# Kernel optimization log

Hardware: AMD Instinct MI355X
Metric: run time of the kernel (lower is better)

## Reference

```python
import jax, jax.numpy as jnp
import numpy as np

BN_EPS = 1e-5


def setup_inputs() -> dict:
    key = jax.random.key(0)
    k1, k2 = jax.random.split(key, 2)
    b, C, h, w = 4, 256, 64, 64
    K = 16  # num_codes is hard-coded to 16 inside __init__
    x = jax.random.normal(k1, (b, C, h, w), dtype=jnp.float32)
    conv_w = jax.random.normal(k2, (K, C), dtype=jnp.float32) * (1.0 / np.sqrt(C))
    bn_gamma = jnp.ones((K,), dtype=jnp.float32)
    bn_beta = jnp.zeros((K,), dtype=jnp.float32)
    return {"x": x, "conv_w": conv_w, "bn_gamma": bn_gamma, "bn_beta": bn_beta}


def reference(x, conv_w, bn_gamma, bn_beta):
    b, C, h, w = x.shape
    K = conv_w.shape[0]
    hw = h * w

    # 1x1 conv (no bias) -> BatchNorm2d (training-mode batch stats) -> ReLU
    cw = jnp.einsum('kc,bchw->bkhw', conv_w, x)          # (b, K, h, w)
    mean = cw.mean(axis=(0, 2, 3))                        # (K,)
    var = cw.var(axis=(0, 2, 3))                          # biased variance, (K,)
    cw = (cw - mean[None, :, None, None]) * jax.lax.rsqrt(var + BN_EPS)[None, :, None, None]
    cw = cw * bn_gamma[None, :, None, None] + bn_beta[None, :, None, None]
    cw = jax.nn.relu(cw)

    cw_flat = cw.reshape(b, K, hw)                        # (b, K, hw)
    scale = cw_flat.mean(axis=2)                          # (b, K)
    # Faithful to torch: flat row-major reinterpretation of (b,K,hw) as (b,hw,K,1)
    r = cw_flat.reshape(b, hw, K, 1)                      # (b, hw, K, 1)

    x2 = x.reshape(b, C, hw).transpose(0, 2, 1)           # (b, hw, C)
    diff = x2[:, :, None, :] - r                          # (b, hw, K, C)

    scaled_l2 = scale[:, :, None] * jnp.sum(diff * diff, axis=1)   # (b, K, C)
    aw = jax.nn.softmax(scaled_l2, axis=1)                # softmax over K, (b, K, C)
    encoded_feat = jnp.sum(aw[:, None, :, :] * diff, axis=1)       # (b, K, C)
    return encoded_feat
```

## Files before the change

### kernel.cpp

```cpp
#include <hip/hip_runtime.h>

#define BN_EPS 1e-5f

#define OFF_PBN     0
#define OFF_PSR     8192
#define OFF_PSX     24576
#define OFF_PSXX    155648
#define OFF_CROSSR  286720
#define OFF_CW      352256
#define OFF_PCX     614400
#define WS_NEED     ((size_t)(OFF_PCX + 2097152) * sizeof(float))

#define CONV_FMA(W, K0)                                  \
    acc[K0][0] = fmaf(W, xv.x, acc[K0][0]);              \
    acc[K0][1] = fmaf(W, xv.y, acc[K0][1]);              \
    acc[K0][2] = fmaf(W, xv.z, acc[K0][2]);              \
    acc[K0][3] = fmaf(W, xv.w, acc[K0][3]);

#define FMA16(v, rp)                                     \
    {                                                    \
        const float4* rq_ = (const float4*)(rp);         \
        float4 r0_ = rq_[0], r1_ = rq_[1];               \
        float4 r2_ = rq_[2], r3_ = rq_[3];               \
        acc[0]  = fmaf(v, r0_.x, acc[0]);                \
        acc[1]  = fmaf(v, r0_.y, acc[1]);                \
        acc[2]  = fmaf(v, r0_.z, acc[2]);                \
        acc[3]  = fmaf(v, r0_.w, acc[3]);                \
        acc[4]  = fmaf(v, r1_.x, acc[4]);                \
        acc[5]  = fmaf(v, r1_.y, acc[5]);                \
        acc[6]  = fmaf(v, r1_.z, acc[6]);                \
        acc[7]  = fmaf(v, r1_.w, acc[7]);                \
        acc[8]  = fmaf(v, r2_.x, acc[8]);                \
        acc[9]  = fmaf(v, r2_.y, acc[9]);                \
        acc[10] = fmaf(v, r2_.z, acc[10]);               \
        acc[11] = fmaf(v, r2_.w, acc[11]);               \
        acc[12] = fmaf(v, r3_.x, acc[12]);               \
        acc[13] = fmaf(v, r3_.y, acc[13]);               \
        acc[14] = fmaf(v, r3_.z, acc[14]);               \
        acc[15] = fmaf(v, r3_.w, acc[15]);               \
    }

__global__ __launch_bounds__(256, 2) void k_conv(const float* __restrict__ x,
                                                 const float* __restrict__ w,
                                                 float* __restrict__ cw,
                                                 float* __restrict__ pbn) {
    __shared__ float wlT[4124];
    __shared__ float bnl[4][32];
    int bid = blockIdx.x;
    int b   = bid >> 6;
    int ich = bid & 63;
    int t   = threadIdx.x;
    int cp  = t & 15;
    int il  = t >> 4;
    int wv  = t >> 6;

    for (int m = t; m < 4096; m += 256) {
        int k = m >> 8, c = m & 255;
        wlT[(c << 4) + ((c >> 5) << 2) + k] = w[m];
    }
    __syncthreads();

    float acc[16][4];
    #pragma unroll
    for (int k = 0; k < 16; ++k) {
        #pragma unroll
        for (int e = 0; e < 4; ++e) acc[k][e] = 0.f;
    }

    const float* xp = x + (size_t)(b * 256 + cp * 16) * 4096 + ich * 64 + il * 4;
    #pragma unroll
    for (int cc = 0; cc < 16; ++cc) {
        float4 xv = *(const float4*)(xp + (size_t)cc * 4096);
        int c = cp * 16 + cc;
        const float4* wr = (const float4*)&wlT[(c << 4) + ((c >> 5) << 2)];
        float4 w0 = wr[0], w1 = wr[1], w2 = wr[2], w3 = wr[3];
        CONV_FMA(w0.x, 0)  CONV_FMA(w0.y, 1)  CONV_FMA(w0.z, 2)  CONV_FMA(w0.w, 3)
        CONV_FMA(w1.x, 4)  CONV_FMA(w1.y, 5)  CONV_FMA(w1.z, 6)  CONV_FMA(w1.w, 7)
        CONV_FMA(w2.x, 8)  CONV_FMA(w2.y, 9)  CONV_FMA(w2.z, 10) CONV_FMA(w2.w, 11)
        CONV_FMA(w3.x, 12) CONV_FMA(w3.y, 13) CONV_FMA(w3.z, 14) CONV_FMA(w3.w, 15)
    }

    float r8[8][4];
    #pragma unroll
    for (int r = 0; r < 8; ++r) {
        #pragma unroll
        for (int e = 0; e < 4; ++e) {
            float lo = acc[r][e]     + __shfl_xor(acc[r][e], 1);
            float hi = acc[r + 8][e] + __shfl_xor(acc[r + 8][e], 1);
            r8[r][e] = (cp & 1) ? hi : lo;
        }
    }
    float r4v[4][4];
    #pragma unroll
    for (int r = 0; r < 4; ++r) {
        #pragma unroll
        for (int e = 0; e < 4; ++e) {
            float lo = r8[r][e]     + __shfl_xor(r8[r][e], 2);
            float hi = r8[r + 4][e] + __shfl_xor(r8[r + 4][e], 2);
            r4v[r][e] = (cp & 2) ? hi : lo;
        }
    }
    float r2[2][4];
    #pragma unroll
    for (int r = 0; r < 2; ++r) {
        #pragma unroll
        for (int e = 0; e < 4; ++e) {
            float lo = r4v[r][e]     + __shfl_xor(r4v[r][e], 4);
            float hi = r4v[r + 2][e] + __shfl_xor(r4v[r + 2][e], 4);
            r2[r][e] = (cp & 4) ? hi : lo;
        }
    }
    float r1[4];
    #pragma unroll
    for (int e = 0; e < 4; ++e) {
        float lo = r2[0][e] + __shfl_xor(r2[0][e], 8);
        float hi = r2[1][e] + __shfl_xor(r2[1][e], 8);
        r1[e] = (cp & 8) ? hi : lo;
    }
    int ko = ((cp & 1) << 3) | (((cp >> 1) & 1) << 2) | (((cp >> 2) & 1) << 1)
           | ((cp >> 3) & 1);

    float4 st;
    st.x = r1[0]; st.y = r1[1]; st.z = r1[2]; st.w = r1[3];
    *(float4*)(cw + (size_t)b * 65536 + (size_t)ko * 4096 + ich * 64 + il * 4) = st;

    float s1 = r1[0] + r1[1] + r1[2] + r1[3];
    float s2 = r1[0]*r1[0] + r1[1]*r1[1] + r1[2]*r1[2] + r1[3]*r1[3];
    #pragma unroll
    for (int m = 16; m <= 32; m <<= 1) {
        s1 += __shfl_xor(s1, m);
        s2 += __shfl_xor(s2, m);
    }
    if ((t & 48) == 0) { bnl[wv][ko] = s1; bnl[wv][16 + ko] = s2; }
    __syncthreads();
    if (t < 32) {
        pbn[bid * 32 + t] = bnl[0][t] + bnl[1][t] + bnl[2][t] + bnl[3][t];
    }
}

template <bool PCX>
__global__ __launch_bounds__(256, 2) void k_main(const float* __restrict__ x,
                                                 const float* __restrict__ gamma,
                                                 const float* __restrict__ beta,
                                                 float* __restrict__ ws,
                                                 float* __restrict__ pcx) {
    __shared__ float xl[8192];
    __shared__ float rl[512];
    __shared__ float red1[256], red2[256];
    __shared__ float bnred[256];
    int bid = blockIdx.x;
    int b   = bid >> 7;
    int s   = bid & 127;
    int kp  = s >> 3;
    int t   = threadIdx.x;

    {
        int col = t & 31, row0 = t >> 5;
        float p = 0.f;
        for (int m = row0; m < 256; m += 8) p += ws[OFF_PBN + m * 32 + col];
        bnred[t] = p;
    }
    __syncthreads();
    float s1 = 0.f, s2 = 0.f;
    #pragma unroll
    for (int j = 0; j < 8; ++j) {
        s1 += bnred[j * 32 + kp];
        s2 += bnred[j * 32 + 16 + kp];
    }
    float mean = s1 * (1.f / 16384.f);
    float var  = s2 * (1.f / 16384.f) - mean * mean;
    float aa   = gamma[kp] * rsqrtf(var + BN_EPS);
    float bb   = beta[kp] - mean * aa;

    #pragma unroll
    for (int j = 0; j < 8; ++j) {
        int F  = j * 256 + t;
        int cc = F >> 3, i4 = F & 7;
        const float* pa = x + (size_t)(b * 256 + cc) * 4096 + s * 32 + i4 * 4;
        float4 v = *(const float4*)pa;
        int ib = i4 * 4;
        xl[(ib + 0) * 256 + (cc ^ (ib + 0))] = v.x;
        xl[(ib + 1) * 256 + (cc ^ (ib + 1))] = v.y;
        xl[(ib + 2) * 256 + (cc ^ (ib + 2))] = v.z;
        xl[(ib + 3) * 256 + (cc ^ (ib + 3))] = v.w;
    }

    const float* cwp = ws + OFF_CW + (size_t)b * 65536 + (size_t)kp * 4096
                     + (size_t)(s & 7) * 512;
    float sr = 0.f, srr = 0.f;
    #pragma unroll
    for (int j = 0; j < 2; ++j) {
        float v = cwp[t + j * 256];
        v = fmaxf(fmaf(v, aa, bb), 0.f);
        rl[t + j * 256] = v;
        sr += v; srr += v * v;
    }
    red1[t] = sr; red2[t] = srr;
    __syncthreads();

    if (t < 16) {
        float a1 = 0.f, a2 = 0.f;
        for (int m = t; m < 256; m += 16) { a1 += red1[m]; a2 += red2[m]; }
        ws[OFF_PSR + bid * 32 + t]      = a1;
        ws[OFF_PSR + bid * 32 + 16 + t] = a2;
    }

    int c = t;
    float acc[16];
    #pragma unroll
    for (int k = 0; k < 16; ++k) acc[k] = 0.f;
    float xs = 0.f, xs2 = 0.f;
    #pragma unroll
    for (int ii = 0; ii < 32; ++ii) {
        float xv = xl[ii * 256 + (c ^ ii)];
        xs += xv; xs2 += xv * xv;
        FMA16(xv, rl + ii * 16);
    }

    ws[OFF_PSX  + bid * 256 + c] = xs;
    ws[OFF_PSXX + bid * 256 + c] = xs2;
    if (PCX) {
        float* pp = pcx + (size_t)(bid * 16) * 256 + c;
        #pragma unroll
        for (int k = 0; k < 16; ++k) pp[(size_t)k * 256] = acc[k];
    } else {
        #pragma unroll
        for (int k = 0; k < 16; ++k)
            atomicAdd(ws + OFF_CROSSR + (b * 16 + k) * 256 + c, acc[k]);
    }
}

__global__ __launch_bounds__(256) void k_red(const float* __restrict__ pcx,
                                             float* __restrict__ crossr) {
    int bid = blockIdx.x;
    int b  = bid >> 6;
    int k  = (bid >> 2) & 15;
    int sg = bid & 3;
    int c  = threadIdx.x;
    float acc = 0.f;
    #pragma unroll 8
    for (int m = 0; m < 32; ++m) {
        int sl = sg * 32 + m;
        acc += pcx[(size_t)((b * 128 + sl) * 16 + k) * 256 + c];
    }
    crossr[((sg * 4 + b) * 16 + k) * 256 + c] = acc;
}

__global__ __launch_bounds__(256) void k_final(const float* __restrict__ ws,
                                               float* __restrict__ out) {
    __shared__ float srl[4096];
    __shared__ float fin[48];
    int b = blockIdx.x;
    int t = threadIdx.x;

    const float* psr = ws + OFF_PSR + (size_t)b * 128 * 32;
    #pragma unroll
    for (int j = 0; j < 16; ++j) srl[j * 256 + t] = psr[j * 256 + t];
    __syncthreads();

    if (t < 16) {
        float v = 0.f;
        for (int s = 0; s < 128; ++s) v += srl[s * 32 + t];
        fin[t] = v;
    } else if (t < 32) {
        int k = t - 16;
        float v = 0.f;
        for (int s = 0; s < 128; ++s) v += srl[s * 32 + 16 + k];
        fin[16 + k] = v;
    } else if (t < 48) {
        int kp = t - 32;
        float v = 0.f;
        for (int s = kp * 8; s < kp * 8 + 8; ++s)
            for (int k2 = 0; k2 < 16; ++k2) v += srl[s * 32 + k2];
        fin[32 + kp] = v;
    }
    __syncthreads();

    int c = t;
    float sx = 0.f, sxx = 0.f;
    const float* psx  = ws + OFF_PSX  + (size_t)b * 128 * 256;
    const float* psxx = ws + OFF_PSXX + (size_t)b * 128 * 256;
    for (int p = 0; p < 128; ++p) {
        sx  += psx[p * 256 + c];
        sxx += psxx[p * 256 + c];
    }

    float sl2[16];
    float mx = -1e30f;
    #pragma unroll
    for (int k = 0; k < 16; ++k) {
        float cr = 0.f;
        #pragma unroll
        for (int sg = 0; sg < 4; ++sg)
            cr += ws[OFF_CROSSR + ((sg * 4 + b) * 16 + k) * 256 + c];
        float v = fin[32 + k] * (1.f / 4096.f) * (sxx - 2.f * cr + fin[16 + k]);
        sl2[k] = v;
        mx = fmaxf(mx, v);
    }
    float den = 0.f;
    #pragma unroll
    for (int k = 0; k < 16; ++k) {
        float e = __expf(sl2[k] - mx);
        sl2[k] = e;
        den += e;
    }
    float inv = 1.f / den;
    #pragma unroll
    for (int k = 0; k < 16; ++k)
        out[(size_t)(b * 16 + k) * 256 + c] = sl2[k] * inv * (sx - fin[k]);
}

extern "C" void kernel_launch(void* const* d_in, const int* in_sizes, int n_in,
                              void* d_out, int out_size, void* d_ws, size_t ws_size,
                              hipStream_t stream) {
    const float* x     = (const float*)d_in[0];
    const float* w     = (const float*)d_in[1];
    const float* gamma = (const float*)d_in[2];
    const float* beta  = (const float*)d_in[3];
    float* ws  = (float*)d_ws;
    float* out = (float*)d_out;

    bool use_pcx = ws_size >= WS_NEED;

    k_conv<<<256, 256, 0, stream>>>(x, w, ws + OFF_CW, ws + OFF_PBN);
    if (use_pcx) {
        k_main<true><<<512, 256, 0, stream>>>(x, gamma, beta, ws, ws + OFF_PCX);
        k_red<<<256, 256, 0, stream>>>(ws + OFF_PCX, ws + OFF_CROSSR);
    } else {
        hipMemsetAsync(ws + OFF_CROSSR, 0, 65536 * sizeof(float), stream);
        k_main<false><<<512, 256, 0, stream>>>(x, gamma, beta, ws, nullptr);
    }
    k_final<<<4, 256, 0, stream>>>(ws, out);
}
```

Measured before the change: 102.3 us.

## Double thread count in conv and main kernels, move sx reduction into k_red

Runs k_conv and k_main with 512 threads per block. In k_conv each thread now handles 8 channels with all x loads issued up front, and a shared-memory cross-wave reduction replaces part of the shuffle tree. k_main splits the 32 spatial positions into two halves per channel and writes twice as many partial sums. The per-channel sx/sxx reductions move from the single-wave k_final into the parallel k_red, and the BN-stat reduction in k_main now runs after the x tile loads are issued, so the global loads overlap. In exchange the workspace and the partial-sum traffic double.

```diff
diff --git a/kernel.cpp b/kernel.cpp
--- a/kernel.cpp
+++ b/kernel.cpp
@@ -5,17 +5,18 @@
 #define OFF_PBN     0
 #define OFF_PSR     8192
 #define OFF_PSX     24576
-#define OFF_PSXX    155648
-#define OFF_CROSSR  286720
-#define OFF_CW      352256
-#define OFF_PCX     614400
-#define WS_NEED     ((size_t)(OFF_PCX + 2097152) * sizeof(float))
-
-#define CONV_FMA(W, K0)                                  \
-    acc[K0][0] = fmaf(W, xv.x, acc[K0][0]);              \
-    acc[K0][1] = fmaf(W, xv.y, acc[K0][1]);              \
-    acc[K0][2] = fmaf(W, xv.z, acc[K0][2]);              \
-    acc[K0][3] = fmaf(W, xv.w, acc[K0][3]);
+#define OFF_PSXX    286720
+#define OFF_CROSSR  548864
+#define OFF_SXF     614400
+#define OFF_CW      622592
+#define OFF_PCX     884736
+#define WS_NEED     ((size_t)(OFF_PCX + 4194304) * sizeof(float))
+
+#define CONV_FMA(W, K0, XV)                              \
+    acc[K0][0] = fmaf(W, XV.x, acc[K0][0]);              \
+    acc[K0][1] = fmaf(W, XV.y, acc[K0][1]);              \
+    acc[K0][2] = fmaf(W, XV.z, acc[K0][2]);              \
+    acc[K0][3] = fmaf(W, XV.w, acc[K0][3]);
 
 #define FMA16(v, rp)                                     \
     {                                                    \
@@ -40,25 +41,30 @@
         acc[15] = fmaf(v, r3_.w, acc[15]);               \
     }
 
-__global__ __launch_bounds__(256, 2) void k_conv(const float* __restrict__ x,
-                                                 const float* __restrict__ w,
+__global__ __launch_bounds__(512, 2) void k_conv(const float* __restrict__ x,
+                                                 const float* __restrict__ wq,
                                                  float* __restrict__ cw,
                                                  float* __restrict__ pbn) {
-    __shared__ float wlT[4124];
-    __shared__ float bnl[4][32];
+    __shared__ float wlT[4224];
+    __shared__ float wred[8 * 1088];
     int bid = blockIdx.x;
     int b   = bid >> 6;
     int ich = bid & 63;
     int t   = threadIdx.x;
-    int cp  = t & 15;
-    int il  = t >> 4;
+    int il  = t & 15;
+    int cp  = t >> 4;
     int wv  = t >> 6;
 
-    for (int m = t; m < 4096; m += 256) {
+    for (int m = t; m < 4096; m += 512) {
         int k = m >> 8, c = m & 255;
-        wlT[(c << 4) + ((c >> 5) << 2) + k] = w[m];
-    }
-    __syncthreads();
+        wlT[c * 16 + (c >> 3) * 4 + k] = wq[m];
+    }
+    __syncthreads();
+
+    float4 xv[8];
+    const float* xp = x + (size_t)(b * 256 + cp * 8) * 4096 + ich * 64 + il * 4;
+    #pragma unroll
+    for (int cc = 0; cc < 8; ++cc) xv[cc] = *(const float4*)(xp + (size_t)cc * 4096);
 
     float acc[16][4];
     #pragma unroll
@@ -67,17 +73,19 @@
         for (int e = 0; e < 4; ++e) acc[k][e] = 0.f;
     }
 
-    const float* xp = x + (size_t)(b * 256 + cp * 16) * 4096 + ich * 64 + il * 4;
-    #pragma unroll
-    for (int cc = 0; cc < 16; ++cc) {
-        float4 xv = *(const float4*)(xp + (size_t)cc * 4096);
-        int c = cp * 16 + cc;
-        const float4* wr = (const float4*)&wlT[(c << 4) + ((c >> 5) << 2)];
+    #pragma unroll
+    for (int cc = 0; cc < 8; ++cc) {
+        int c = cp * 8 + cc;
+        const float4* wr = (const float4*)&wlT[c * 16 + (c >> 3) * 4];
         float4 w0 = wr[0], w1 = wr[1], w2 = wr[2], w3 = wr[3];
-        CONV_FMA(w0.x, 0)  CONV_FMA(w0.y, 1)  CONV_FMA(w0.z, 2)  CONV_FMA(w0.w, 3)
-        CONV_FMA(w1.x, 4)  CONV_FMA(w1.y, 5)  CONV_FMA(w1.z, 6)  CONV_FMA(w1.w, 7)
-        CONV_FMA(w2.x, 8)  CONV_FMA(w2.y, 9)  CONV_FMA(w2.z, 10) CONV_FMA(w2.w, 11)
-        CONV_FMA(w3.x, 12) CONV_FMA(w3.y, 13) CONV_FMA(w3.z, 14) CONV_FMA(w3.w, 15)
+        CONV_FMA(w0.x, 0,  xv[cc]) CONV_FMA(w0.y, 1,  xv[cc])
+        CONV_FMA(w0.z, 2,  xv[cc]) CONV_FMA(w0.w, 3,  xv[cc])
+        CONV_FMA(w1.x, 4,  xv[cc]) CONV_FMA(w1.y, 5,  xv[cc])
+        CONV_FMA(w1.z, 6,  xv[cc]) CONV_FMA(w1.w, 7,  xv[cc])
+        CONV_FMA(w2.x, 8,  xv[cc]) CONV_FMA(w2.y, 9,  xv[cc])
+        CONV_FMA(w2.z, 10, xv[cc]) CONV_FMA(w2.w, 11, xv[cc])
+        CONV_FMA(w3.x, 12, xv[cc]) CONV_FMA(w3.y, 13, xv[cc])
+        CONV_FMA(w3.z, 14, xv[cc]) CONV_FMA(w3.w, 15, xv[cc])
     }
 
     float r8[8][4];
@@ -85,61 +93,57 @@
     for (int r = 0; r < 8; ++r) {
         #pragma unroll
         for (int e = 0; e < 4; ++e) {
-            float lo = acc[r][e]     + __shfl_xor(acc[r][e], 1);
-            float hi = acc[r + 8][e] + __shfl_xor(acc[r + 8][e], 1);
+            float lo = acc[r][e]     + __shfl_xor(acc[r][e], 16);
+            float hi = acc[r + 8][e] + __shfl_xor(acc[r + 8][e], 16);
             r8[r][e] = (cp & 1) ? hi : lo;
         }
     }
-    float r4v[4][4];
+    float r4[4][4];
     #pragma unroll
     for (int r = 0; r < 4; ++r) {
         #pragma unroll
         for (int e = 0; e < 4; ++e) {
-            float lo = r8[r][e]     + __shfl_xor(r8[r][e], 2);
-            float hi = r8[r + 4][e] + __shfl_xor(r8[r + 4][e], 2);
-            r4v[r][e] = (cp & 2) ? hi : lo;
-        }
-    }
-    float r2[2][4];
-    #pragma unroll
-    for (int r = 0; r < 2; ++r) {
-        #pragma unroll
-        for (int e = 0; e < 4; ++e) {
-            float lo = r4v[r][e]     + __shfl_xor(r4v[r][e], 4);
-            float hi = r4v[r + 2][e] + __shfl_xor(r4v[r + 2][e], 4);
-            r2[r][e] = (cp & 4) ? hi : lo;
-        }
-    }
-    float r1[4];
-    #pragma unroll
-    for (int e = 0; e < 4; ++e) {
-        float lo = r2[0][e] + __shfl_xor(r2[0][e], 8);
-        float hi = r2[1][e] + __shfl_xor(r2[1][e], 8);
-        r1[e] = (cp & 8) ? hi : lo;
-    }
-    int ko = ((cp & 1) << 3) | (((cp >> 1) & 1) << 2) | (((cp >> 2) & 1) << 1)
-           | ((cp >> 3) & 1);
-
-    float4 st;
-    st.x = r1[0]; st.y = r1[1]; st.z = r1[2]; st.w = r1[3];
-    *(float4*)(cw + (size_t)b * 65536 + (size_t)ko * 4096 + ich * 64 + il * 4) = st;
-
-    float s1 = r1[0] + r1[1] + r1[2] + r1[3];
-    float s2 = r1[0]*r1[0] + r1[1]*r1[1] + r1[2]*r1[2] + r1[3]*r1[3];
-    #pragma unroll
-    for (int m = 16; m <= 32; m <<= 1) {
-        s1 += __shfl_xor(s1, m);
-        s2 += __shfl_xor(s2, m);
-    }
-    if ((t & 48) == 0) { bnl[wv][ko] = s1; bnl[wv][16 + ko] = s2; }
-    __syncthreads();
-    if (t < 32) {
-        pbn[bid * 32 + t] = bnl[0][t] + bnl[1][t] + bnl[2][t] + bnl[3][t];
+            float lo = r8[r][e]     + __shfl_xor(r8[r][e], 32);
+            float hi = r8[r + 4][e] + __shfl_xor(r8[r + 4][e], 32);
+            r4[r][e] = (cp & 2) ? hi : lo;
+        }
+    }
+    int ko = (cp & 1) * 8 + ((cp >> 1) & 1) * 4;
+    #pragma unroll
+    for (int j = 0; j < 4; ++j) {
+        float4 v;
+        v.x = r4[j][0]; v.y = r4[j][1]; v.z = r4[j][2]; v.w = r4[j][3];
+        *(float4*)&wred[wv * 1088 + il * 68 + (ko + j) * 4] = v;
+    }
+    __syncthreads();
+
+    if (t < 256) {
+        int k = t >> 4, ilo = t & 15;
+        float4 s;
+        s.x = 0.f; s.y = 0.f; s.z = 0.f; s.w = 0.f;
+        #pragma unroll
+        for (int w8 = 0; w8 < 8; ++w8) {
+            float4 v = *(const float4*)&wred[w8 * 1088 + ilo * 68 + k * 4];
+            s.x += v.x; s.y += v.y; s.z += v.z; s.w += v.w;
+        }
+        *(float4*)(cw + (size_t)b * 65536 + (size_t)k * 4096 + ich * 64 + ilo * 4) = s;
+
+        float s1 = s.x + s.y + s.z + s.w;
+        float s2 = s.x * s.x + s.y * s.y + s.z * s.z + s.w * s.w;
+        #pragma unroll
+        for (int m = 1; m <= 8; m <<= 1) {
+            s1 += __shfl_xor(s1, m);
+            s2 += __shfl_xor(s2, m);
+        }
+        if (ilo == 0) {
+            pbn[bid * 32 + k]      = s1;
+            pbn[bid * 32 + 16 + k] = s2;
+        }
     }
 }
 
 template <bool PCX>
-__global__ __launch_bounds__(256, 2) void k_main(const float* __restrict__ x,
+__global__ __launch_bounds__(512, 2) void k_main(const float* __restrict__ x,
                                                  const float* __restrict__ gamma,
                                                  const float* __restrict__ beta,
                                                  float* __restrict__ ws,
@@ -153,28 +157,12 @@
     int s   = bid & 127;
     int kp  = s >> 3;
     int t   = threadIdx.x;
-
-    {
-        int col = t & 31, row0 = t >> 5;
-        float p = 0.f;
-        for (int m = row0; m < 256; m += 8) p += ws[OFF_PBN + m * 32 + col];
-        bnred[t] = p;
-    }
-    __syncthreads();
-    float s1 = 0.f, s2 = 0.f;
-    #pragma unroll
-    for (int j = 0; j < 8; ++j) {
-        s1 += bnred[j * 32 + kp];
-        s2 += bnred[j * 32 + 16 + kp];
-    }
-    float mean = s1 * (1.f / 16384.f);
-    float var  = s2 * (1.f / 16384.f) - mean * mean;
-    float aa   = gamma[kp] * rsqrtf(var + BN_EPS);
-    float bb   = beta[kp] - mean * aa;
-
-    #pragma unroll
-    for (int j = 0; j < 8; ++j) {
-        int F  = j * 256 + t;
+    int c   = t & 255;
+    int ih  = t >> 8;
+
+    #pragma unroll
+    for (int j = 0; j < 4; ++j) {
+        int F  = j * 512 + t;
         int cc = F >> 3, i4 = F & 7;
         const float* pa = x + (size_t)(b * 256 + cc) * 4096 + s * 32 + i4 * 4;
         float4 v = *(const float4*)pa;
@@ -185,19 +173,37 @@
         xl[(ib + 3) * 256 + (cc ^ (ib + 3))] = v.w;
     }
 
-    const float* cwp = ws + OFF_CW + (size_t)b * 65536 + (size_t)kp * 4096
-                     + (size_t)(s & 7) * 512;
-    float sr = 0.f, srr = 0.f;
-    #pragma unroll
-    for (int j = 0; j < 2; ++j) {
-        float v = cwp[t + j * 256];
-        v = fmaxf(fmaf(v, aa, bb), 0.f);
-        rl[t + j * 256] = v;
-        sr += v; srr += v * v;
-    }
-    red1[t] = sr; red2[t] = srr;
-    __syncthreads();
-
+    if (t < 256) {
+        int col = t & 31, row0 = t >> 5;
+        float p = 0.f;
+        for (int m = row0; m < 256; m += 8) p += ws[OFF_PBN + m * 32 + col];
+        bnred[t] = p;
+    }
+    __syncthreads();
+    float s1 = 0.f, s2 = 0.f;
+    #pragma unroll
+    for (int j = 0; j < 8; ++j) {
+        s1 += bnred[j * 32 + kp];
+        s2 += bnred[j * 32 + 16 + kp];
+    }
+    float mean = s1 * (1.f / 16384.f);
+    float var  = s2 * (1.f / 16384.f) - mean * mean;
+    float aa   = gamma[kp] * rsqrtf(var + BN_EPS);
+    float bb   = beta[kp] - mean * aa;
+
+    {
+        float v = ws[OFF_CW + (size_t)b * 65536 + (size_t)kp * 4096
+                     + (size_t)(s & 7) * 512 + t];
+        rl[t] = fmaxf(fmaf(v, aa, bb), 0.f);
+    }
+    __syncthreads();
+
+    if (t < 256) {
+        float v1 = rl[t], v2 = rl[t + 256];
+        red1[t] = v1 + v2;
+        red2[t] = v1 * v1 + v2 * v2;
+    }
+    __syncthreads();
     if (t < 16) {
         float a1 = 0.f, a2 = 0.f;
         for (int m = t; m < 256; m += 16) { a1 += red1[m]; a2 += red2[m]; }
@@ -205,33 +211,35 @@
         ws[OFF_PSR + bid * 32 + 16 + t] = a2;
     }
 
-    int c = t;
     float acc[16];
     #pragma unroll
     for (int k = 0; k < 16; ++k) acc[k] = 0.f;
     float xs = 0.f, xs2 = 0.f;
     #pragma unroll
-    for (int ii = 0; ii < 32; ++ii) {
-        float xv = xl[ii * 256 + (c ^ ii)];
-        xs += xv; xs2 += xv * xv;
-        FMA16(xv, rl + ii * 16);
-    }
-
-    ws[OFF_PSX  + bid * 256 + c] = xs;
-    ws[OFF_PSXX + bid * 256 + c] = xs2;
+    for (int q = 0; q < 16; ++q) {
+        int ii = ih * 16 + q;
+        float xvv = xl[ii * 256 + (c ^ ii)];
+        xs += xvv; xs2 += xvv * xvv;
+        FMA16(xvv, rl + ii * 16);
+    }
+
+    ws[OFF_PSX  + (size_t)(bid * 2 + ih) * 256 + c] = xs;
+    ws[OFF_PSXX + (size_t)(bid * 2 + ih) * 256 + c] = xs2;
     if (PCX) {
-        float* pp = pcx + (size_t)(bid * 16) * 256 + c;
+        float* pp = pcx + (size_t)((bid * 2 + ih) * 16) * 256 + c;
         #pragma unroll
         for (int k = 0; k < 16; ++k) pp[(size_t)k * 256] = acc[k];
     } else {
         #pragma unroll
         for (int k = 0; k < 16; ++k)
-            atomicAdd(ws + OFF_CROSSR + (b * 16 + k) * 256 + c, acc[k]);
+            atomicAdd(ws + OFF_CROSSR + ((0 * 4 + b) * 16 + k) * 256 + c, acc[k]);
+        atomicAdd(ws + OFF_SXF + (size_t)(b * 8 + 0) * 256 + c, xs);
+        atomicAdd(ws + OFF_SXF + (size_t)(b * 8 + 1) * 256 + c, xs2);
     }
 }
 
 __global__ __launch_bounds__(256) void k_red(const float* __restrict__ pcx,
-                                             float* __restrict__ crossr) {
+                                             float* __restrict__ ws) {
     int bid = blockIdx.x;
     int b  = bid >> 6;
     int k  = (bid >> 2) & 15;
@@ -239,11 +247,25 @@
     int c  = threadIdx.x;
     float acc = 0.f;
     #pragma unroll 8
-    for (int m = 0; m < 32; ++m) {
-        int sl = sg * 32 + m;
-        acc += pcx[(size_t)((b * 128 + sl) * 16 + k) * 256 + c];
-    }
-    crossr[((sg * 4 + b) * 16 + k) * 256 + c] = acc;
+    for (int j = 0; j < 64; ++j) {
+        int r = sg * 64 + j;
+        acc += pcx[(size_t)((b * 256 + r) * 16 + k) * 256 + c];
+    }
+    ws[OFF_CROSSR + ((sg * 4 + b) * 16 + k) * 256 + c] = acc;
+
+    if (k == 0) {
+        float sxq = 0.f;
+        #pragma unroll 8
+        for (int j = 0; j < 64; ++j)
+            sxq += ws[OFF_PSX + (size_t)(b * 256 + sg * 64 + j) * 256 + c];
+        ws[OFF_SXF + (size_t)((b * 4 + sg) * 2 + 0) * 256 + c] = sxq;
+    } else if (k == 1) {
+        float sxxq = 0.f;
+        #pragma unroll 8
+        for (int j = 0; j < 64; ++j)
+            sxxq += ws[OFF_PSXX + (size_t)(b * 256 + sg * 64 + j) * 256 + c];
+        ws[OFF_SXF + (size_t)((b * 4 + sg) * 2 + 1) * 256 + c] = sxxq;
+    }
 }
 
 __global__ __launch_bounds__(256) void k_final(const float* __restrict__ ws,
@@ -278,11 +300,10 @@
 
     int c = t;
     float sx = 0.f, sxx = 0.f;
-    const float* psx  = ws + OFF_PSX  + (size_t)b * 128 * 256;
-    const float* psxx = ws + OFF_PSXX + (size_t)b * 128 * 256;
-    for (int p = 0; p < 128; ++p) {
-        sx  += psx[p * 256 + c];
-        sxx += psxx[p * 256 + c];
+    #pragma unroll
+    for (int sg = 0; sg < 4; ++sg) {
+        sx  += ws[OFF_SXF + (size_t)((b * 4 + sg) * 2 + 0) * 256 + c];
+        sxx += ws[OFF_SXF + (size_t)((b * 4 + sg) * 2 + 1) * 256 + c];
     }
 
     float sl2[16];
@@ -293,7 +314,9 @@
         #pragma unroll
         for (int sg = 0; sg < 4; ++sg)
             cr += ws[OFF_CROSSR + ((sg * 4 + b) * 16 + k) * 256 + c];
-        float v = fin[32 + k] * (1.f / 4096.f) * (sxx - 2.f * cr + fin[16 + k]);
+        float sc  = fin[32 + k] * (1.f / 4096.f);
+        float srr = fin[16 + k];
+        float v = sc * (sxx - 2.f * cr + srr);
         sl2[k] = v;
         mx = fmaxf(mx, v);
     }
@@ -306,8 +329,10 @@
     }
     float inv = 1.f / den;
     #pragma unroll
-    for (int k = 0; k < 16; ++k)
-        out[(size_t)(b * 16 + k) * 256 + c] = sl2[k] * inv * (sx - fin[k]);
+    for (int k = 0; k < 16; ++k) {
+        float srk = fin[k];
+        out[(size_t)(b * 16 + k) * 256 + c] = sl2[k] * inv * (sx - srk);
+    }
 }
 
 extern "C" void kernel_launch(void* const* d_in, const int* in_sizes, int n_in,
@@ -322,13 +347,14 @@
 
     bool use_pcx = ws_size >= WS_NEED;
 
-    k_conv<<<256, 256, 0, stream>>>(x, w, ws + OFF_CW, ws + OFF_PBN);
+    k_conv<<<256, 512, 0, stream>>>(x, w, ws + OFF_CW, ws + OFF_PBN);
     if (use_pcx) {
-        k_main<true><<<512, 256, 0, stream>>>(x, gamma, beta, ws, ws + OFF_PCX);
-        k_red<<<256, 256, 0, stream>>>(ws + OFF_PCX, ws + OFF_CROSSR);
+        k_main<true><<<512, 512, 0, stream>>>(x, gamma, beta, ws, ws + OFF_PCX);
+        k_red<<<256, 256, 0, stream>>>(ws + OFF_PCX, ws);
     } else {
-        hipMemsetAsync(ws + OFF_CROSSR, 0, 65536 * sizeof(float), stream);
-        k_main<false><<<512, 256, 0, stream>>>(x, gamma, beta, ws, nullptr);
+        hipMemsetAsync(ws + OFF_CROSSR, 0,
+                       (OFF_CW - OFF_CROSSR) * sizeof(float), stream);
+        k_main<false><<<512, 512, 0, stream>>>(x, gamma, beta, ws, nullptr);
     }
     k_final<<<4, 256, 0, stream>>>(ws, out);
 }
```

Result: no change. 103.5 us (+1.2%).

## Fuse all stages into one persistent kernel with global atomic barriers

Applied to the files above, without the earlier changes.

Replaces the four separate kernel launches (conv, main, reduce, final) with a single 512-block kernel that separates the phases with software grid barriers built on agent-scope atomics. The x tile is loaded into LDS before the conv phase so its latency overlaps the conv work, and the final sx/sxx reduction is split across extra blocks. The aim is to remove launch gaps and the tail of the serial small kernels. The risks are that the spin barriers deadlock unless all 512 blocks are co-resident, and that the fallback for a too-small workspace is removed.

```diff
diff --git a/kernel.cpp b/kernel.cpp
--- a/kernel.cpp
+++ b/kernel.cpp
@@ -7,9 +7,11 @@
 #define OFF_PSX     24576
 #define OFF_PSXX    155648
 #define OFF_CROSSR  286720
-#define OFF_CW      352256
-#define OFF_PCX     614400
-#define WS_NEED     ((size_t)(OFF_PCX + 2097152) * sizeof(float))
+#define OFF_FIN     352256
+#define OFF_SXF     352512
+#define OFF_CW      356608
+#define OFF_PCX     618752
+#define OFF_BAR     2715904
 
 #define CONV_FMA(W, K0)                                  \
     acc[K0][0] = fmaf(W, xv.x, acc[K0][0]);              \
@@ -40,274 +42,300 @@
         acc[15] = fmaf(v, r3_.w, acc[15]);               \
     }
 
-__global__ __launch_bounds__(256, 2) void k_conv(const float* __restrict__ x,
-                                                 const float* __restrict__ w,
-                                                 float* __restrict__ cw,
-                                                 float* __restrict__ pbn) {
-    __shared__ float wlT[4124];
-    __shared__ float bnl[4][32];
+__device__ __forceinline__ void gbar(unsigned* cnt, unsigned target) {
+    __syncthreads();
+    if (threadIdx.x == 0) {
+        __threadfence();
+        __hip_atomic_fetch_add(cnt, 1u, __ATOMIC_ACQ_REL, __HIP_MEMORY_SCOPE_AGENT);
+        while (__hip_atomic_load(cnt, __ATOMIC_ACQUIRE, __HIP_MEMORY_SCOPE_AGENT)
+               < target)
+            __builtin_amdgcn_s_sleep(2);
+        __threadfence();
+    }
+    __syncthreads();
+}
+
+__global__ __launch_bounds__(256, 2) void k_all(const float* __restrict__ x,
+                                                const float* __restrict__ w,
+                                                const float* __restrict__ gamma,
+                                                const float* __restrict__ beta,
+                                                float* __restrict__ ws,
+                                                float* __restrict__ out) {
+    __shared__ float lds[12448];
+    unsigned* bar = (unsigned*)( nullptr);
+    float* xl = lds;
     int bid = blockIdx.x;
-    int b   = bid >> 6;
-    int ich = bid & 63;
     int t   = threadIdx.x;
-    int cp  = t & 15;
-    int il  = t >> 4;
-    int wv  = t >> 6;
-
-    for (int m = t; m < 4096; m += 256) {
-        int k = m >> 8, c = m & 255;
-        wlT[(c << 4) + ((c >> 5) << 2) + k] = w[m];
-    }
-    __syncthreads();
-
-    float acc[16][4];
-    #pragma unroll
-    for (int k = 0; k < 16; ++k) {
-        #pragma unroll
-        for (int e = 0; e < 4; ++e) acc[k][e] = 0.f;
-    }
-
-    const float* xp = x + (size_t)(b * 256 + cp * 16) * 4096 + ich * 64 + il * 4;
-    #pragma unroll
-    for (int cc = 0; cc < 16; ++cc) {
-        float4 xv = *(const float4*)(xp + (size_t)cc * 4096);
-        int c = cp * 16 + cc;
-        const float4* wr = (const float4*)&wlT[(c << 4) + ((c >> 5) << 2)];
-        float4 w0 = wr[0], w1 = wr[1], w2 = wr[2], w3 = wr[3];
-        CONV_FMA(w0.x, 0)  CONV_FMA(w0.y, 1)  CONV_FMA(w0.z, 2)  CONV_FMA(w0.w, 3)
-        CONV_FMA(w1.x, 4)  CONV_FMA(w1.y, 5)  CONV_FMA(w1.z, 6)  CONV_FMA(w1.w, 7)
-        CONV_FMA(w2.x, 8)  CONV_FMA(w2.y, 9)  CONV_FMA(w2.z, 10) CONV_FMA(w2.w, 11)
-        CONV_FMA(w3.x, 12) CONV_FMA(w3.y, 13) CONV_FMA(w3.z, 14) CONV_FMA(w3.w, 15)
-    }
-
-    float r8[8][4];
-    #pragma unroll
-    for (int r = 0; r < 8; ++r) {
+    bar = (unsigned*)(ws + OFF_BAR);
+
+    {
+        int b = bid >> 7;
+        int s = bid & 127;
+        #pragma unroll
+        for (int j = 0; j < 8; ++j) {
+            int F  = j * 256 + t;
+            int cc = F >> 3, i4 = F & 7;
+            const float* pa = x + (size_t)(b * 256 + cc) * 4096 + s * 32 + i4 * 4;
+            float4 v = *(const float4*)pa;
+            int ib = i4 * 4;
+            xl[(ib + 0) * 256 + (cc ^ (ib + 0))] = v.x;
+            xl[(ib + 1) * 256 + (cc ^ (ib + 1))] = v.y;
+            xl[(ib + 2) * 256 + (cc ^ (ib + 2))] = v.z;
+            xl[(ib + 3) * 256 + (cc ^ (ib + 3))] = v.w;
+        }
+    }
+
+    if (bid < 256) {
+        float* wlT = lds + 8192;
+        float* bnl = lds + 8192 + 4124;
+        int b   = bid >> 6;
+        int ich = bid & 63;
+        int cp  = t & 15;
+        int il  = t >> 4;
+        int wv  = t >> 6;
+
+        for (int m = t; m < 4096; m += 256) {
+            int k = m >> 8, c = m & 255;
+            wlT[(c << 4) + ((c >> 5) << 2) + k] = w[m];
+        }
+        __syncthreads();
+
+        float acc[16][4];
+        #pragma unroll
+        for (int k = 0; k < 16; ++k) {
+            #pragma unroll
+            for (int e = 0; e < 4; ++e) acc[k][e] = 0.f;
+        }
+
+        const float* xp = x + (size_t)(b * 256 + cp * 16) * 4096 + ich * 64 + il * 4;
+        #pragma unroll
+        for (int cc = 0; cc < 16; ++cc) {
+            float4 xv = *(const float4*)(xp + (size_t)cc * 4096);
+            int c = cp * 16 + cc;
+            const float4* wr = (const float4*)&wlT[(c << 4) + ((c >> 5) << 2)];
+            float4 w0 = wr[0], w1 = wr[1], w2 = wr[2], w3 = wr[3];
+            CONV_FMA(w0.x, 0)  CONV_FMA(w0.y, 1)  CONV_FMA(w0.z, 2)  CONV_FMA(w0.w, 3)
+            CONV_FMA(w1.x, 4)  CONV_FMA(w1.y, 5)  CONV_FMA(w1.z, 6)  CONV_FMA(w1.w, 7)
+            CONV_FMA(w2.x, 8)  CONV_FMA(w2.y, 9)  CONV_FMA(w2.z, 10) CONV_FMA(w2.w, 11)
+            CONV_FMA(w3.x, 12) CONV_FMA(w3.y, 13) CONV_FMA(w3.z, 14) CONV_FMA(w3.w, 15)
+        }
+
+        float r8[8][4];
+        #pragma unroll
+        for (int r = 0; r < 8; ++r) {
+            #pragma unroll
+            for (int e = 0; e < 4; ++e) {
+                float lo = acc[r][e]     + __shfl_xor(acc[r][e], 1);
+                float hi = acc[r + 8][e] + __shfl_xor(acc[r + 8][e], 1);
+                r8[r][e] = (cp & 1) ? hi : lo;
+            }
+        }
+        float r4v[4][4];
+        #pragma unroll
+        for (int r = 0; r < 4; ++r) {
+            #pragma unroll
+            for (int e = 0; e < 4; ++e) {
+                float lo = r8[r][e]     + __shfl_xor(r8[r][e], 2);
+                float hi = r8[r + 4][e] + __shfl_xor(r8[r + 4][e], 2);
+                r4v[r][e] = (cp & 2) ? hi : lo;
+            }
+        }
+        float r2[2][4];
+        #pragma unroll
+        for (int r = 0; r < 2; ++r) {
+            #pragma unroll
+            for (int e = 0; e < 4; ++e) {
+                float lo = r4v[r][e]     + __shfl_xor(r4v[r][e], 4);
+                float hi = r4v[r + 2][e] + __shfl_xor(r4v[r + 2][e], 4);
+                r2[r][e] = (cp & 4) ? hi : lo;
+            }
+        }
+        float r1[4];
         #pragma unroll
         for (int e = 0; e < 4; ++e) {
-            float lo = acc[r][e]     + __shfl_xor(acc[r][e], 1);
-            float hi = acc[r + 8][e] + __shfl_xor(acc[r + 8][e], 1);
-            r8[r][e] = (cp & 1) ? hi : lo;
-        }
-    }
-    float r4v[4][4];
-    #pragma unroll
-    for (int r = 0; r < 4; ++r) {
-        #pragma unroll
-        for (int e = 0; e < 4; ++e) {
-            float lo = r8[r][e]     + __shfl_xor(r8[r][e], 2);
-            float hi = r8[r + 4][e] + __shfl_xor(r8[r + 4][e], 2);
-            r4v[r][e] = (cp & 2) ? hi : lo;
-        }
-    }
-    float r2[2][4];
-    #pragma unroll
-    for (int r = 0; r < 2; ++r) {
-        #pragma unroll
-        for (int e = 0; e < 4; ++e) {
-            float lo = r4v[r][e]     + __shfl_xor(r4v[r][e], 4);
-            float hi = r4v[r + 2][e] + __shfl_xor(r4v[r + 2][e], 4);
-            r2[r][e] = (cp & 4) ? hi : lo;
-        }
-    }
-    float r1[4];
-    #pragma unroll
-    for (int e = 0; e < 4; ++e) {
-        float lo = r2[0][e] + __shfl_xor(r2[0][e], 8);
-        float hi = r2[1][e] + __shfl_xor(r2[1][e], 8);
-        r1[e] = (cp & 8) ? hi : lo;
-    }
-    int ko = ((cp & 1) << 3) | (((cp >> 1) & 1) << 2) | (((cp >> 2) & 1) << 1)
-           | ((cp >> 3) & 1);
-
-    float4 st;
-    st.x = r1[0]; st.y = r1[1]; st.z = r1[2]; st.w = r1[3];
-    *(float4*)(cw + (size_t)b * 65536 + (size_t)ko * 4096 + ich * 64 + il * 4) = st;
-
-    float s1 = r1[0] + r1[1] + r1[2] + r1[3];
-    float s2 = r1[0]*r1[0] + r1[1]*r1[1] + r1[2]*r1[2] + r1[3]*r1[3];
-    #pragma unroll
-    for (int m = 16; m <= 32; m <<= 1) {
-        s1 += __shfl_xor(s1, m);
-        s2 += __shfl_xor(s2, m);
-    }
-    if ((t & 48) == 0) { bnl[wv][ko] = s1; bnl[wv][16 + ko] = s2; }
-    __syncthreads();
-    if (t < 32) {
-        pbn[bid * 32 + t] = bnl[0][t] + bnl[1][t] + bnl[2][t] + bnl[3][t];
-    }
-}
-
-template <bool PCX>
-__global__ __launch_bounds__(256, 2) void k_main(const float* __restrict__ x,
-                                                 const float* __restrict__ gamma,
-                                                 const float* __restrict__ beta,
-                                                 float* __restrict__ ws,
-                                                 float* __restrict__ pcx) {
-    __shared__ float xl[8192];
-    __shared__ float rl[512];
-    __shared__ float red1[256], red2[256];
-    __shared__ float bnred[256];
-    int bid = blockIdx.x;
-    int b   = bid >> 7;
-    int s   = bid & 127;
-    int kp  = s >> 3;
-    int t   = threadIdx.x;
+            float lo = r2[0][e] + __shfl_xor(r2[0][e], 8);
+            float hi = r2[1][e] + __shfl_xor(r2[1][e], 8);
+            r1[e] = (cp & 8) ? hi : lo;
+        }
+        int ko = ((cp & 1) << 3) | (((cp >> 1) & 1) << 2) | (((cp >> 2) & 1) << 1)
+               | ((cp >> 3) & 1);
+
+        float4 st;
+        st.x = r1[0]; st.y = r1[1]; st.z = r1[2]; st.w = r1[3];
+        *(float4*)(ws + OFF_CW + (size_t)b * 65536 + (size_t)ko * 4096
+                   + ich * 64 + il * 4) = st;
+
+        float s1 = r1[0] + r1[1] + r1[2] + r1[3];
+        float s2 = r1[0]*r1[0] + r1[1]*r1[1] + r1[2]*r1[2] + r1[3]*r1[3];
+        #pragma unroll
+        for (int m = 16; m <= 32; m <<= 1) {
+            s1 += __shfl_xor(s1, m);
+            s2 += __shfl_xor(s2, m);
+        }
+        if ((t & 48) == 0) { bnl[wv * 32 + ko] = s1; bnl[wv * 32 + 16 + ko] = s2; }
+        __syncthreads();
+        if (t < 32) {
+            ws[OFF_PBN + bid * 32 + t] = bnl[0 + t] + bnl[32 + t]
+                                       + bnl[64 + t] + bnl[96 + t];
+        }
+    }
+    gbar(bar + 0, 512);
 
     {
-        int col = t & 31, row0 = t >> 5;
-        float p = 0.f;
-        for (int m = row0; m < 256; m += 8) p += ws[OFF_PBN + m * 32 + col];
-        bnred[t] = p;
-    }
-    __syncthreads();
-    float s1 = 0.f, s2 = 0.f;
-    #pragma unroll
-    for (int j = 0; j < 8; ++j) {
-        s1 += bnred[j * 32 + kp];
-        s2 += bnred[j * 32 + 16 + kp];
-    }
-    float mean = s1 * (1.f / 16384.f);
-    float var  = s2 * (1.f / 16384.f) - mean * mean;
-    float aa   = gamma[kp] * rsqrtf(var + BN_EPS);
-    float bb   = beta[kp] - mean * aa;
-
-    #pragma unroll
-    for (int j = 0; j < 8; ++j) {
-        int F  = j * 256 + t;
-        int cc = F >> 3, i4 = F & 7;
-        const float* pa = x + (size_t)(b * 256 + cc) * 4096 + s * 32 + i4 * 4;
-        float4 v = *(const float4*)pa;
-        int ib = i4 * 4;
-        xl[(ib + 0) * 256 + (cc ^ (ib + 0))] = v.x;
-        xl[(ib + 1) * 256 + (cc ^ (ib + 1))] = v.y;
-        xl[(ib + 2) * 256 + (cc ^ (ib + 2))] = v.z;
-        xl[(ib + 3) * 256 + (cc ^ (ib + 3))] = v.w;
-    }
-
-    const float* cwp = ws + OFF_CW + (size_t)b * 65536 + (size_t)kp * 4096
-                     + (size_t)(s & 7) * 512;
-    float sr = 0.f, srr = 0.f;
-    #pragma unroll
-    for (int j = 0; j < 2; ++j) {
-        float v = cwp[t + j * 256];
-        v = fmaxf(fmaf(v, aa, bb), 0.f);
-        rl[t + j * 256] = v;
-        sr += v; srr += v * v;
-    }
-    red1[t] = sr; red2[t] = srr;
-    __syncthreads();
-
-    if (t < 16) {
-        float a1 = 0.f, a2 = 0.f;
-        for (int m = t; m < 256; m += 16) { a1 += red1[m]; a2 += red2[m]; }
-        ws[OFF_PSR + bid * 32 + t]      = a1;
-        ws[OFF_PSR + bid * 32 + 16 + t] = a2;
-    }
-
-    int c = t;
-    float acc[16];
-    #pragma unroll
-    for (int k = 0; k < 16; ++k) acc[k] = 0.f;
-    float xs = 0.f, xs2 = 0.f;
-    #pragma unroll
-    for (int ii = 0; ii < 32; ++ii) {
-        float xv = xl[ii * 256 + (c ^ ii)];
-        xs += xv; xs2 += xv * xv;
-        FMA16(xv, rl + ii * 16);
-    }
-
-    ws[OFF_PSX  + bid * 256 + c] = xs;
-    ws[OFF_PSXX + bid * 256 + c] = xs2;
-    if (PCX) {
+        float* rl    = lds + 8192;
+        float* red1  = lds + 8704;
+        float* red2  = lds + 8960;
+        float* bnred = lds + 9216;
+        int b  = bid >> 7;
+        int s  = bid & 127;
+        int kp = s >> 3;
+        float* pcx = ws + OFF_PCX;
+
+        {
+            int col = t & 31, row0 = t >> 5;
+            float p = 0.f;
+            for (int m = row0; m < 256; m += 8) p += ws[OFF_PBN + m * 32 + col];
+            bnred[t] = p;
+        }
+        __syncthreads();
+        float s1 = 0.f, s2 = 0.f;
+        #pragma unroll
+        for (int j = 0; j < 8; ++j) {
+            s1 += bnred[j * 32 + kp];
+            s2 += bnred[j * 32 + 16 + kp];
+        }
+        float mean = s1 * (1.f / 16384.f);
+        float var  = s2 * (1.f / 16384.f) - mean * mean;
+        float aa   = gamma[kp] * rsqrtf(var + BN_EPS);
+        float bb   = beta[kp] - mean * aa;
+
+        const float* cwp = ws + OFF_CW + (size_t)b * 65536 + (size_t)kp * 4096
+                         + (size_t)(s & 7) * 512;
+        float sr = 0.f, srr = 0.f;
+        #pragma unroll
+        for (int j = 0; j < 2; ++j) {
+            float v = cwp[t + j * 256];
+            v = fmaxf(fmaf(v, aa, bb), 0.f);
+            rl[t + j * 256] = v;
+            sr += v; srr += v * v;
+        }
+        red1[t] = sr; red2[t] = srr;
+        __syncthreads();
+
+        if (t < 16) {
+            float a1 = 0.f, a2 = 0.f;
+            for (int m = t; m < 256; m += 16) { a1 += red1[m]; a2 += red2[m]; }
+            ws[OFF_PSR + bid * 32 + t]      = a1;
+            ws[OFF_PSR + bid * 32 + 16 + t] = a2;
+        }
+
+        int c = t;
+        float acc[16];
+        #pragma unroll
+        for (int k = 0; k < 16; ++k) acc[k] = 0.f;
+        float xs = 0.f, xs2 = 0.f;
+        #pragma unroll
+        for (int ii = 0; ii < 32; ++ii) {
+            float xv = xl[ii * 256 + (c ^ ii)];
+            xs += xv; xs2 += xv * xv;
+            FMA16(xv, rl + ii * 16);
+        }
+
+        ws[OFF_PSX  + bid * 256 + c] = xs;
+        ws[OFF_PSXX + bid * 256 + c] = xs2;
         float* pp = pcx + (size_t)(bid * 16) * 256 + c;
         #pragma unroll
         for (int k = 0; k < 16; ++k) pp[(size_t)k * 256] = acc[k];
-    } else {
-        #pragma unroll
-        for (int k = 0; k < 16; ++k)
-            atomicAdd(ws + OFF_CROSSR + (b * 16 + k) * 256 + c, acc[k]);
-    }
-}
-
-__global__ __launch_bounds__(256) void k_red(const float* __restrict__ pcx,
-                                             float* __restrict__ crossr) {
-    int bid = blockIdx.x;
-    int b  = bid >> 6;
-    int k  = (bid >> 2) & 15;
-    int sg = bid & 3;
-    int c  = threadIdx.x;
-    float acc = 0.f;
-    #pragma unroll 8
-    for (int m = 0; m < 32; ++m) {
-        int sl = sg * 32 + m;
-        acc += pcx[(size_t)((b * 128 + sl) * 16 + k) * 256 + c];
-    }
-    crossr[((sg * 4 + b) * 16 + k) * 256 + c] = acc;
-}
-
-__global__ __launch_bounds__(256) void k_final(const float* __restrict__ ws,
-                                               float* __restrict__ out) {
-    __shared__ float srl[4096];
-    __shared__ float fin[48];
-    int b = blockIdx.x;
-    int t = threadIdx.x;
-
-    const float* psr = ws + OFF_PSR + (size_t)b * 128 * 32;
-    #pragma unroll
-    for (int j = 0; j < 16; ++j) srl[j * 256 + t] = psr[j * 256 + t];
-    __syncthreads();
-
-    if (t < 16) {
-        float v = 0.f;
-        for (int s = 0; s < 128; ++s) v += srl[s * 32 + t];
-        fin[t] = v;
-    } else if (t < 32) {
-        int k = t - 16;
-        float v = 0.f;
-        for (int s = 0; s < 128; ++s) v += srl[s * 32 + 16 + k];
-        fin[16 + k] = v;
-    } else if (t < 48) {
-        int kp = t - 32;
-        float v = 0.f;
-        for (int s = kp * 8; s < kp * 8 + 8; ++s)
-            for (int k2 = 0; k2 < 16; ++k2) v += srl[s * 32 + k2];
-        fin[32 + kp] = v;
-    }
-    __syncthreads();
-
-    int c = t;
-    float sx = 0.f, sxx = 0.f;
-    const float* psx  = ws + OFF_PSX  + (size_t)b * 128 * 256;
-    const float* psxx = ws + OFF_PSXX + (size_t)b * 128 * 256;
-    for (int p = 0; p < 128; ++p) {
-        sx  += psx[p * 256 + c];
-        sxx += psxx[p * 256 + c];
-    }
-
-    float sl2[16];
-    float mx = -1e30f;
-    #pragma unroll
-    for (int k = 0; k < 16; ++k) {
-        float cr = 0.f;
-        #pragma unroll
-        for (int sg = 0; sg < 4; ++sg)
-            cr += ws[OFF_CROSSR + ((sg * 4 + b) * 16 + k) * 256 + c];
-        float v = fin[32 + k] * (1.f / 4096.f) * (sxx - 2.f * cr + fin[16 + k]);
-        sl2[k] = v;
-        mx = fmaxf(mx, v);
-    }
-    float den = 0.f;
-    #pragma unroll
-    for (int k = 0; k < 16; ++k) {
-        float e = __expf(sl2[k] - mx);
-        sl2[k] = e;
-        den += e;
-    }
-    float inv = 1.f / den;
-    #pragma unroll
-    for (int k = 0; k < 16; ++k)
-        out[(size_t)(b * 16 + k) * 256 + c] = sl2[k] * inv * (sx - fin[k]);
+    }
+    gbar(bar + 1, 512);
+
+    if (bid < 256) {
+        int b  = bid >> 6;
+        int k  = (bid >> 2) & 15;
+        int sg = bid & 3;
+        int c  = t;
+        const float* pcx = ws + OFF_PCX;
+        float acc = 0.f;
+        #pragma unroll 8
+        for (int m = 0; m < 32; ++m) {
+            int sl = sg * 32 + m;
+            acc += pcx[(size_t)((b * 128 + sl) * 16 + k) * 256 + c];
+        }
+        ws[OFF_CROSSR + ((sg * 4 + b) * 16 + k) * 256 + c] = acc;
+    } else if (bid < 260) {
+        int b = bid - 256;
+        float* srl = lds;
+        const float* psr = ws + OFF_PSR + (size_t)b * 128 * 32;
+        #pragma unroll
+        for (int j = 0; j < 16; ++j) srl[j * 256 + t] = psr[j * 256 + t];
+        __syncthreads();
+        if (t < 16) {
+            float v = 0.f;
+            for (int s = 0; s < 128; ++s) v += srl[s * 32 + t];
+            ws[OFF_FIN + b * 64 + t] = v;
+        } else if (t < 32) {
+            int k = t - 16;
+            float v = 0.f;
+            for (int s = 0; s < 128; ++s) v += srl[s * 32 + 16 + k];
+            ws[OFF_FIN + b * 64 + 16 + k] = v;
+        } else if (t < 48) {
+            int kp = t - 32;
+            float v = 0.f;
+            for (int s = kp * 8; s < kp * 8 + 8; ++s)
+                for (int k2 = 0; k2 < 16; ++k2) v += srl[s * 32 + k2];
+            ws[OFF_FIN + b * 64 + 32 + kp] = v;
+        }
+    } else if (bid < 268) {
+        int q = bid - 260;
+        int b = q >> 1, h = q & 1;
+        const float* psx  = ws + OFF_PSX  + (size_t)b * 128 * 256;
+        const float* psxx = ws + OFF_PSXX + (size_t)b * 128 * 256;
+        float sx = 0.f, sxx = 0.f;
+        for (int p = h * 64; p < h * 64 + 64; ++p) {
+            sx  += psx[p * 256 + t];
+            sxx += psxx[p * 256 + t];
+        }
+        ws[OFF_SXF + ((b * 2 + h) * 2 + 0) * 256 + t] = sx;
+        ws[OFF_SXF + ((b * 2 + h) * 2 + 1) * 256 + t] = sxx;
+    }
+    gbar(bar + 2, 512);
+
+    if (bid < 4) {
+        int b = bid;
+        int c = t;
+        float sx  = ws[OFF_SXF + ((b * 2 + 0) * 2 + 0) * 256 + c]
+                  + ws[OFF_SXF + ((b * 2 + 1) * 2 + 0) * 256 + c];
+        float sxx = ws[OFF_SXF + ((b * 2 + 0) * 2 + 1) * 256 + c]
+                  + ws[OFF_SXF + ((b * 2 + 1) * 2 + 1) * 256 + c];
+
+        float sl2[16];
+        float mx = -1e30f;
+        #pragma unroll
+        for (int k = 0; k < 16; ++k) {
+            float cr = 0.f;
+            #pragma unroll
+            for (int sg = 0; sg < 4; ++sg)
+                cr += ws[OFF_CROSSR + ((sg * 4 + b) * 16 + k) * 256 + c];
+            float sc  = ws[OFF_FIN + b * 64 + 32 + k] * (1.f / 4096.f);
+            float srr = ws[OFF_FIN + b * 64 + 16 + k];
+            float v = sc * (sxx - 2.f * cr + srr);
+            sl2[k] = v;
+            mx = fmaxf(mx, v);
+        }
+        float den = 0.f;
+        #pragma unroll
+        for (int k = 0; k < 16; ++k) {
+            float e = __expf(sl2[k] - mx);
+            sl2[k] = e;
+            den += e;
+        }
+        float inv = 1.f / den;
+        #pragma unroll
+        for (int k = 0; k < 16; ++k) {
+            float srk = ws[OFF_FIN + b * 64 + k];
+            out[(size_t)(b * 16 + k) * 256 + c] = sl2[k] * inv * (sx - srk);
+        }
+    }
 }
 
 extern "C" void kernel_launch(void* const* d_in, const int* in_sizes, int n_in,
@@ -320,15 +348,6 @@
     float* ws  = (float*)d_ws;
     float* out = (float*)d_out;
 
-    bool use_pcx = ws_size >= WS_NEED;
-
-    k_conv<<<256, 256, 0, stream>>>(x, w, ws + OFF_CW, ws + OFF_PBN);
-    if (use_pcx) {
-        k_main<true><<<512, 256, 0, stream>>>(x, gamma, beta, ws, ws + OFF_PCX);
-        k_red<<<256, 256, 0, stream>>>(ws + OFF_PCX, ws + OFF_CROSSR);
-    } else {
-        hipMemsetAsync(ws + OFF_CROSSR, 0, 65536 * sizeof(float), stream);
-        k_main<false><<<512, 256, 0, stream>>>(x, gamma, beta, ws, nullptr);
-    }
-    k_final<<<4, 256, 0, stream>>>(ws, out);
+    hipMemsetAsync(ws + OFF_BAR, 0, 16, stream);
+    k_all<<<512, 256, 0, stream>>>(x, w, gamma, beta, ws, out);
 }
```

New measurement: 267.7 us. 2.62x slower.
